# Performance work log

Measured on AMD Instinct MI355X. Metric: run time of the kernel, lower is better.

The kernel has to match this reference:

```python
import jax, jax.numpy as jnp
import numpy as np

N_NODES = 40000
N_EDGES = 320000
IN_C = 256
OUT_C = 256
K = 5


def setup_inputs() -> dict:
    key = jax.random.key(0)
    k1, k2, k3, k4, k5 = jax.random.split(key, 5)
    x = jax.random.normal(k1, (N_NODES, IN_C), dtype=jnp.float32)
    edge_index = jax.random.randint(k2, (2, N_EDGES), 0, N_NODES, dtype=jnp.int64)
    edge_weight = jax.random.uniform(k3, (N_EDGES,), dtype=jnp.float32)
    # parameters: uniform(-stdv, stdv) with stdv = 1/sqrt(in_channels * K)
    stdv = 1.0 / np.sqrt(IN_C * K)
    weight = jax.random.uniform(k4, (K, IN_C, OUT_C), dtype=jnp.float32,
                                minval=-stdv, maxval=stdv)
    bias = jax.random.uniform(k5, (OUT_C,), dtype=jnp.float32,
                              minval=-stdv, maxval=stdv)
    return {"x": x, "edge_index": edge_index, "edge_weight": edge_weight,
            "weight": weight, "bias": bias}


def reference(x, edge_index, edge_weight, weight, bias):
    row, col = edge_index[0], edge_index[1]
    num_nodes = x.shape[0]
    k_order = weight.shape[0]

    # remove_self_loops: mask out row==col edges (static-shape equivalent)
    keep = (row != col)
    ew = jnp.where(keep, edge_weight, 0.0)

    # degree over rows (counting only non-self-loop edges), D^{-1/2}
    deg = jax.ops.segment_sum(keep.astype(x.dtype), row, num_segments=num_nodes)
    deg_inv_sqrt = jnp.where(deg > 0, jax.lax.rsqrt(jnp.maximum(deg, 1.0)), 0.0)

    # scaled Laplacian edge values: -d_r^{-1/2} * w * d_c^{-1/2}
    lap = -deg_inv_sqrt[row] * ew * deg_inv_sqrt[col]

    def spmm(v):  # [N, C] -> [N, C] : scatter-add of lap-weighted gathered rows
        return jax.ops.segment_sum(lap[:, None] * v[col], row, num_segments=num_nodes)

    # Chebyshev recursion: T0 = x, T1 = L x, T_k = 2 L T_{k-1} - T_{k-2}
    tx0 = x
    out = tx0 @ weight[0]
    if k_order > 1:
        tx1 = spmm(x)
        out = out + tx1 @ weight[1]
        for k in range(2, k_order):
            tx2 = 2.0 * spmm(tx1) - tx0
            out = out + tx2 @ weight[k]
            tx0, tx1 = tx1, tx2
    return out + bias
```

## Files before the change

kernel.cpp:

```cpp
#include <hip/hip_runtime.h>

#define NN 40000
#define NE 320000
#define C 256
#define KORD 5
#define KT 1280

typedef __attribute__((ext_vector_type(8))) short short8;
typedef __attribute__((ext_vector_type(4))) float floatx4;
typedef unsigned short bf16_t;
typedef unsigned long long u64;

__device__ __forceinline__ bf16_t f2bf(float f) {
    union { float f; unsigned u; } v; v.f = f;
    unsigned r = v.u + 0x7fffu + ((v.u >> 16) & 1u);
    return (bf16_t)(r >> 16);
}
__device__ __forceinline__ float bf2f(bf16_t h) {
    union { unsigned u; float f; } v; v.u = ((unsigned)h) << 16;
    return v.f;
}

#define GLL16(gsrc, ldst)                                                        \
    __builtin_amdgcn_global_load_lds(                                            \
        (const __attribute__((address_space(1))) void*)(gsrc),                   \
        (__attribute__((address_space(3))) void*)(ldst), 16, 0, 0)

__global__ __launch_bounds__(256)
void mega0_kernel(const int* __restrict__ ei,
                  int* __restrict__ self_cnt,
                  const float* __restrict__ x, bf16_t* __restrict__ abf,
                  const float* __restrict__ W, bf16_t* __restrict__ WT) {
    int bid = blockIdx.x, t = threadIdx.x;
    if (bid < 1250) {
        int e = bid * 256 + t;
        int r = ei[e];
        int c = ei[NE + e];
        atomicAdd(&self_cnt[NN + r], 1);
        if (r == c) atomicAdd(&self_cnt[r], 1);
    } else if (bid < 11250) {
        int i = (bid - 1250) * 256 + t;
        int n = i >> 6, cg = i & 63;
        float4 f = *(const float4*)&x[(size_t)n * C + cg * 4];
        ushort4 h;
        h.x = f2bf(f.x); h.y = f2bf(f.y); h.z = f2bf(f.z); h.w = f2bf(f.w);
        *(ushort4*)&abf[(size_t)n * KT + cg * 4] = h;
    } else {
        int i = (bid - 11250) * 256 + t;
        int n = i & 255, kt = i >> 8;
        WT[(size_t)n * KT + kt] = f2bf(W[(size_t)kt * 256 + n]);
    }
}

__global__ void scan1_kernel(const int* __restrict__ cnt,
                             int* __restrict__ incl,
                             int* __restrict__ bsum) {
    __shared__ int s[256];
    int t = threadIdx.x;
    int idx = blockIdx.x * 256 + t;
    int v = (idx < NN) ? cnt[idx] : 0;
    s[t] = v;
    __syncthreads();
    for (int off = 1; off < 256; off <<= 1) {
        int add = (t >= off) ? s[t - off] : 0;
        __syncthreads();
        s[t] += add;
        __syncthreads();
    }
    if (idx < NN) incl[idx] = s[t];
    if (t == 255) bsum[blockIdx.x] = s[255];
}

__global__ void scan3_kernel(const int* __restrict__ self_cnt,
                             const int* __restrict__ incl,
                             const int* __restrict__ bsum,
                             float* __restrict__ dis,
                             int* __restrict__ row_ptr,
                             int* __restrict__ cursor) {
    __shared__ int ws[4];
    int bid = blockIdx.x, t = threadIdx.x;
    int v = (t < bid) ? bsum[t] : 0;
#pragma unroll
    for (int off = 32; off >= 1; off >>= 1) v += __shfl_down(v, off);
    if ((t & 63) == 0) ws[t >> 6] = v;
    __syncthreads();
    int bexcl = ws[0] + ws[1] + ws[2] + ws[3];
    int idx = bid * 256 + t;
    if (idx == 0) row_ptr[NN] = NE;
    if (idx >= NN) return;
    int cv = self_cnt[NN + idx];
    int rp = incl[idx] - cv + bexcl;
    row_ptr[idx] = rp;
    cursor[idx]  = rp;
    int d = cv - self_cnt[idx];
    dis[idx] = (d > 0) ? rsqrtf((float)d) : 0.0f;
}

__global__ void fill_kernel(const int* __restrict__ ei,
                            const float* __restrict__ ew,
                            const float* __restrict__ dis,
                            int* __restrict__ cursor,
                            u64* __restrict__ csr) {
    int e = blockIdx.x * 256 + threadIdx.x;
    if (e >= NE) return;
    int r = ei[e];
    int c = ei[NE + e];
    int pos = atomicAdd(&cursor[r], 1);
    float w = (r != c) ? ew[e] : 0.0f;
    float v = -dis[r] * w * dis[c];
    union { float f; unsigned u; } vb; vb.f = v;
    csr[pos] = ((u64)vb.u << 32) | (unsigned)c;
}

__global__ __launch_bounds__(256)
void spmm_kernel(const bf16_t* __restrict__ Vb,
                 const bf16_t* __restrict__ subb,
                 const int* __restrict__ row_ptr,
                 const u64* __restrict__ csr,
                 bf16_t* __restrict__ outb,
                 float alpha, int use_sub) {
    int wave = __builtin_amdgcn_readfirstlane(threadIdx.x >> 6);
    int lane = threadIdx.x & 63;
    int n = blockIdx.x * 4 + wave;
    int j0 = row_ptr[n];
    int j1 = row_ptr[n + 1];
    int cb = lane * 4;
    float a0 = 0.f, a1 = 0.f, a2 = 0.f, a3 = 0.f;
    int j = j0;
    for (; j + 8 <= j1; j += 8) {
        u64 pp[8]; ushort4 vv[8];
#pragma unroll
        for (int u = 0; u < 8; ++u) pp[u] = csr[j + u];
#pragma unroll
        for (int u = 0; u < 8; ++u)
            vv[u] = *(const ushort4*)&Vb[(size_t)(unsigned)(pp[u] & 0xffffffffu) * KT + cb];
#pragma unroll
        for (int u = 0; u < 8; ++u) {
            union { unsigned u; float f; } wb; wb.u = (unsigned)(pp[u] >> 32);
            float w = wb.f;
            a0 += w * bf2f(vv[u].x); a1 += w * bf2f(vv[u].y);
            a2 += w * bf2f(vv[u].z); a3 += w * bf2f(vv[u].w);
        }
    }
    for (; j + 4 <= j1; j += 4) {
        u64 pp[4]; ushort4 vv[4];
#pragma unroll
        for (int u = 0; u < 4; ++u) pp[u] = csr[j + u];
#pragma unroll
        for (int u = 0; u < 4; ++u)
            vv[u] = *(const ushort4*)&Vb[(size_t)(unsigned)(pp[u] & 0xffffffffu) * KT + cb];
#pragma unroll
        for (int u = 0; u < 4; ++u) {
            union { unsigned u; float f; } wb; wb.u = (unsigned)(pp[u] >> 32);
            float w = wb.f;
            a0 += w * bf2f(vv[u].x); a1 += w * bf2f(vv[u].y);
            a2 += w * bf2f(vv[u].z); a3 += w * bf2f(vv[u].w);
        }
    }
    for (; j < j1; ++j) {
        u64 pk = csr[j];
        union { unsigned u; float f; } wb; wb.u = (unsigned)(pk >> 32);
        float w = wb.f;
        ushort4 v = *(const ushort4*)&Vb[(size_t)(unsigned)(pk & 0xffffffffu) * KT + cb];
        a0 += w * bf2f(v.x); a1 += w * bf2f(v.y);
        a2 += w * bf2f(v.z); a3 += w * bf2f(v.w);
    }
    float r0, r1, r2, r3;
    if (use_sub) {
        ushort4 s = *(const ushort4*)&subb[(size_t)n * KT + cb];
        r0 = alpha * a0 - bf2f(s.x);
        r1 = alpha * a1 - bf2f(s.y);
        r2 = alpha * a2 - bf2f(s.z);
        r3 = alpha * a3 - bf2f(s.w);
    } else {
        r0 = alpha * a0; r1 = alpha * a1; r2 = alpha * a2; r3 = alpha * a3;
    }
    ushort4 h;
    h.x = f2bf(r0); h.y = f2bf(r1); h.z = f2bf(r2); h.w = f2bf(r3);
    *(ushort4*)&outb[(size_t)n * KT + cb] = h;
}

__global__ __launch_bounds__(256, 2)
void gemm_mfma(const bf16_t* __restrict__ Abf,
               const bf16_t* __restrict__ WT,
               const float* __restrict__ bias,
               float* __restrict__ out) {
    __shared__ bf16_t smem[3][12288];
    int tid = threadIdx.x;
    int w = tid >> 6, lane = tid & 63;
    int m0 = blockIdx.x * 64;
    int n0 = blockIdx.y * 128;
    int wm = w & 1, wn = w >> 1;
    int quad = lane >> 4, l16 = lane & 15, l7 = l16 & 7;

    const bf16_t* srcbase[6];
#pragma unroll
    for (int j = 0; j < 6; ++j) {
        int gi = (w * 6 + j) * 64 + lane;
        int isB = gi >= 512;
        int t  = isB ? gi - 512 : gi;
        int row = t >> 3;
        int pg = t & 7;
        int g  = pg ^ (row & 7);
        srcbase[j] = (isB ? WT + (size_t)(n0 + row) * KT
                          : Abf + (size_t)(m0 + row) * KT) + g * 8;
    }

    int arowb = wm * 32 + l16;
    int browb = wn * 64 + l16;

    floatx4 acc[2][4] = {};

    const int NT = KT / 64;

#pragma unroll
    for (int j = 0; j < 6; ++j)
        GLL16(srcbase[j] + 0 * 64, &smem[0][(w * 6 + j) * 512]);
#pragma unroll
    for (int j = 0; j < 6; ++j)
        GLL16(srcbase[j] + 1 * 64, &smem[1][(w * 6 + j) * 512]);

    int bufc = 0;
    for (int t = 0; t < NT; ++t) {
        if (t < NT - 1) {
            asm volatile("s_waitcnt vmcnt(6)" ::: "memory");
        } else {
            asm volatile("s_waitcnt vmcnt(0)" ::: "memory");
        }
        __builtin_amdgcn_sched_barrier(0);
        __builtin_amdgcn_s_barrier();

        if (t + 2 < NT) {
            int bnext = bufc + 2; if (bnext >= 3) bnext -= 3;
#pragma unroll
            for (int j = 0; j < 6; ++j)
                GLL16(srcbase[j] + (t + 2) * 64, &smem[bnext][(w * 6 + j) * 512]);
        }

        const bf16_t* sb = smem[bufc];
#pragma unroll
        for (int c = 0; c < 2; ++c) {
            int gp   = (c * 4 + quad) ^ l7;
            int aoff = (arowb * 8 + gp) * 8;
            int boff = 4096 + (browb * 8 + gp) * 8;
            short8 af[2], bfr[4];
#pragma unroll
            for (int mt = 0; mt < 2; ++mt) af[mt]  = *(const short8*)&sb[aoff + mt * 1024];
#pragma unroll
            for (int nt = 0; nt < 4; ++nt) bfr[nt] = *(const short8*)&sb[boff + nt * 1024];
#pragma unroll
            for (int mt = 0; mt < 2; ++mt)
#pragma unroll
                for (int nt = 0; nt < 4; ++nt)
                    acc[mt][nt] = __builtin_amdgcn_mfma_f32_16x16x32_bf16(
                        af[mt], bfr[nt], acc[mt][nt], 0, 0, 0);
        }

        bufc += 1; if (bufc == 3) bufc = 0;
    }

#pragma unroll
    for (int nt = 0; nt < 4; ++nt) {
        int n = n0 + wn * 64 + nt * 16 + l16;
        float bv = bias[n];
#pragma unroll
        for (int mt = 0; mt < 2; ++mt) {
            int mbase = m0 + wm * 32 + mt * 16 + quad * 4;
#pragma unroll
            for (int r = 0; r < 4; ++r)
                out[(size_t)(mbase + r) * C + n] = acc[mt][nt][r] + bv;
        }
    }
}


extern "C" void kernel_launch(void* const* d_in, const int* in_sizes, int n_in,
                              void* d_out, int out_size, void* d_ws, size_t ws_size,
                              hipStream_t stream) {
    const float* x    = (const float*)d_in[0];
    const int*   ei   = (const int*)d_in[1];
    const float* ew   = (const float*)d_in[2];
    const float* W    = (const float*)d_in[3];
    const float* bias = (const float*)d_in[4];
    float* out = (float*)d_out;

    char* p = (char*)d_ws;
    auto carve = [&](size_t bytes) {
        char* q = p;
        p += (bytes + 255) & ~(size_t)255;
        return q;
    };
    int*    self_cnt = (int*)  carve(NN * 4 * 2);
    int*    incl    = (int*)   carve(NN * 4);
    int*    bsum    = (int*)   carve(256 * 4);
    int*    row_ptr = (int*)   carve((NN + 1) * 4);
    int*    cursor  = (int*)   carve(NN * 4);
    u64*    csr     = (u64*)   carve((size_t)NE * 8);
    float*  dis     = (float*) carve(NN * 4);
    bf16_t* abf     = (bf16_t*)carve((size_t)NN * KT * 2);
    bf16_t* WT      = (bf16_t*)carve((size_t)C * KT * 2);
    (void)ws_size; (void)n_in; (void)in_sizes; (void)out_size;

    const int NB_E = (NE + 255) / 256;
    const int NB_N = (NN + 255) / 256;

    hipMemsetAsync(self_cnt, 0, NN * 4 * 2, stream);

    mega0_kernel<<<12530, 256, 0, stream>>>(ei, self_cnt, x, abf, W, WT);

    scan1_kernel<<<NB_N, 256, 0, stream>>>(self_cnt + NN, incl, bsum);
    scan3_kernel<<<NB_N, 256, 0, stream>>>(self_cnt, incl, bsum, dis, row_ptr, cursor);
    fill_kernel<<<NB_E, 256, 0, stream>>>(ei, ew, dis, cursor, csr);

    spmm_kernel<<<NN / 4, 256, 0, stream>>>(abf + 0 * 256, nullptr, row_ptr, csr,
                                            abf + 1 * 256, 1.0f, 0);
    spmm_kernel<<<NN / 4, 256, 0, stream>>>(abf + 1 * 256, abf + 0 * 256, row_ptr,
                                            csr, abf + 2 * 256, 2.0f, 1);
    spmm_kernel<<<NN / 4, 256, 0, stream>>>(abf + 2 * 256, abf + 1 * 256, row_ptr,
                                            csr, abf + 3 * 256, 2.0f, 1);
    spmm_kernel<<<NN / 4, 256, 0, stream>>>(abf + 3 * 256, abf + 2 * 256, row_ptr,
                                            csr, abf + 4 * 256, 2.0f, 1);

    dim3 ggrid(625, 2);
    gemm_mfma<<<ggrid, 256, 0, stream>>>(abf, WT, bias, out);
}
```

Measured before the change: 282.2 us.

## Replace CSR build with fixed-width ELL layout and drop scan kernels

Replaces the count/scan/fill CSR construction with a fixed-width ELL array of 40 slots per row, indexed directly by row and an atomic cursor. This removes the two scan kernels and the row_ptr and dis arrays; the normalisation factors are now computed inside the fill kernel from the degree counts. The SpMM loop now always runs in steps of 8 over zero-padded slots (zero weight, column 0), so the remainder loops go away. In exchange, a larger workspace region (about 12.8 MB) must be memset each call, each row does some wasted padded gathers, and any row with more than 40 edges would overflow silently into the next row.

New measurement: 278.7 us. About the same (-1.3%).

```diff
diff --git a/kernel.cpp b/kernel.cpp
--- a/kernel.cpp
+++ b/kernel.cpp
@@ -5,6 +5,7 @@
 #define C 256
 #define KORD 5
 #define KT 1280
+#define ELLW 40
 
 typedef __attribute__((ext_vector_type(8))) short short8;
 typedef __attribute__((ext_vector_type(4))) float floatx4;
@@ -28,7 +29,7 @@
 
 __global__ __launch_bounds__(256)
 void mega0_kernel(const int* __restrict__ ei,
-                  int* __restrict__ self_cnt,
+                  int* __restrict__ self, int* __restrict__ cntA,
                   const float* __restrict__ x, bf16_t* __restrict__ abf,
                   const float* __restrict__ W, bf16_t* __restrict__ WT) {
     int bid = blockIdx.x, t = threadIdx.x;
@@ -36,8 +37,8 @@
         int e = bid * 256 + t;
         int r = ei[e];
         int c = ei[NE + e];
-        atomicAdd(&self_cnt[NN + r], 1);
-        if (r == c) atomicAdd(&self_cnt[r], 1);
+        atomicAdd(&cntA[r], 1);
+        if (r == c) atomicAdd(&self[r], 1);
     } else if (bid < 11250) {
         int i = (bid - 1250) * 256 + t;
         int n = i >> 6, cg = i & 63;
@@ -52,85 +53,46 @@
     }
 }
 
-__global__ void scan1_kernel(const int* __restrict__ cnt,
-                             int* __restrict__ incl,
-                             int* __restrict__ bsum) {
-    __shared__ int s[256];
-    int t = threadIdx.x;
-    int idx = blockIdx.x * 256 + t;
-    int v = (idx < NN) ? cnt[idx] : 0;
-    s[t] = v;
-    __syncthreads();
-    for (int off = 1; off < 256; off <<= 1) {
-        int add = (t >= off) ? s[t - off] : 0;
-        __syncthreads();
-        s[t] += add;
-        __syncthreads();
-    }
-    if (idx < NN) incl[idx] = s[t];
-    if (t == 255) bsum[blockIdx.x] = s[255];
-}
-
-__global__ void scan3_kernel(const int* __restrict__ self_cnt,
-                             const int* __restrict__ incl,
-                             const int* __restrict__ bsum,
-                             float* __restrict__ dis,
-                             int* __restrict__ row_ptr,
-                             int* __restrict__ cursor) {
-    __shared__ int ws[4];
-    int bid = blockIdx.x, t = threadIdx.x;
-    int v = (t < bid) ? bsum[t] : 0;
-#pragma unroll
-    for (int off = 32; off >= 1; off >>= 1) v += __shfl_down(v, off);
-    if ((t & 63) == 0) ws[t >> 6] = v;
-    __syncthreads();
-    int bexcl = ws[0] + ws[1] + ws[2] + ws[3];
-    int idx = bid * 256 + t;
-    if (idx == 0) row_ptr[NN] = NE;
-    if (idx >= NN) return;
-    int cv = self_cnt[NN + idx];
-    int rp = incl[idx] - cv + bexcl;
-    row_ptr[idx] = rp;
-    cursor[idx]  = rp;
-    int d = cv - self_cnt[idx];
-    dis[idx] = (d > 0) ? rsqrtf((float)d) : 0.0f;
-}
-
-__global__ void fill_kernel(const int* __restrict__ ei,
-                            const float* __restrict__ ew,
-                            const float* __restrict__ dis,
-                            int* __restrict__ cursor,
-                            u64* __restrict__ csr) {
+__global__ __launch_bounds__(256)
+void fill_kernel(const int* __restrict__ ei,
+                 const float* __restrict__ ew,
+                 const int* __restrict__ self,
+                 const int* __restrict__ cntA,
+                 int* __restrict__ cur,
+                 u64* __restrict__ ell) {
     int e = blockIdx.x * 256 + threadIdx.x;
     if (e >= NE) return;
     int r = ei[e];
     int c = ei[NE + e];
-    int pos = atomicAdd(&cursor[r], 1);
+    int pos = atomicAdd(&cur[r], 1);
     float w = (r != c) ? ew[e] : 0.0f;
-    float v = -dis[r] * w * dis[c];
+    int dgr = cntA[r] - self[r];
+    int dgc = cntA[c] - self[c];
+    float dr = (dgr > 0) ? rsqrtf((float)dgr) : 0.0f;
+    float dc = (dgc > 0) ? rsqrtf((float)dgc) : 0.0f;
+    float v = -dr * w * dc;
     union { float f; unsigned u; } vb; vb.f = v;
-    csr[pos] = ((u64)vb.u << 32) | (unsigned)c;
+    ell[(size_t)r * ELLW + pos] = ((u64)vb.u << 32) | (unsigned)c;
 }
 
 __global__ __launch_bounds__(256)
 void spmm_kernel(const bf16_t* __restrict__ Vb,
                  const bf16_t* __restrict__ subb,
-                 const int* __restrict__ row_ptr,
-                 const u64* __restrict__ csr,
+                 const int* __restrict__ cntA,
+                 const u64* __restrict__ ell,
                  bf16_t* __restrict__ outb,
                  float alpha, int use_sub) {
     int wave = __builtin_amdgcn_readfirstlane(threadIdx.x >> 6);
     int lane = threadIdx.x & 63;
     int n = blockIdx.x * 4 + wave;
-    int j0 = row_ptr[n];
-    int j1 = row_ptr[n + 1];
+    const u64* row = ell + (size_t)n * ELLW;
+    int jmax = (cntA[n] + 7) & ~7;
     int cb = lane * 4;
     float a0 = 0.f, a1 = 0.f, a2 = 0.f, a3 = 0.f;
-    int j = j0;
-    for (; j + 8 <= j1; j += 8) {
+    for (int j = 0; j < jmax; j += 8) {
         u64 pp[8]; ushort4 vv[8];
 #pragma unroll
-        for (int u = 0; u < 8; ++u) pp[u] = csr[j + u];
+        for (int u = 0; u < 8; ++u) pp[u] = row[j + u];
 #pragma unroll
         for (int u = 0; u < 8; ++u)
             vv[u] = *(const ushort4*)&Vb[(size_t)(unsigned)(pp[u] & 0xffffffffu) * KT + cb];
@@ -141,29 +103,6 @@
             a0 += w * bf2f(vv[u].x); a1 += w * bf2f(vv[u].y);
             a2 += w * bf2f(vv[u].z); a3 += w * bf2f(vv[u].w);
         }
-    }
-    for (; j + 4 <= j1; j += 4) {
-        u64 pp[4]; ushort4 vv[4];
-#pragma unroll
-        for (int u = 0; u < 4; ++u) pp[u] = csr[j + u];
-#pragma unroll
-        for (int u = 0; u < 4; ++u)
-            vv[u] = *(const ushort4*)&Vb[(size_t)(unsigned)(pp[u] & 0xffffffffu) * KT + cb];
-#pragma unroll
-        for (int u = 0; u < 4; ++u) {
-            union { unsigned u; float f; } wb; wb.u = (unsigned)(pp[u] >> 32);
-            float w = wb.f;
-            a0 += w * bf2f(vv[u].x); a1 += w * bf2f(vv[u].y);
-            a2 += w * bf2f(vv[u].z); a3 += w * bf2f(vv[u].w);
-        }
-    }
-    for (; j < j1; ++j) {
-        u64 pk = csr[j];
-        union { unsigned u; float f; } wb; wb.u = (unsigned)(pk >> 32);
-        float w = wb.f;
-        ushort4 v = *(const ushort4*)&Vb[(size_t)(unsigned)(pk & 0xffffffffu) * KT + cb];
-        a0 += w * bf2f(v.x); a1 += w * bf2f(v.y);
-        a2 += w * bf2f(v.z); a3 += w * bf2f(v.w);
     }
     float r0, r1, r2, r3;
     if (use_sub) {
@@ -290,36 +229,30 @@
         p += (bytes + 255) & ~(size_t)255;
         return q;
     };
-    int*    self_cnt = (int*)  carve(NN * 4 * 2);
-    int*    incl    = (int*)   carve(NN * 4);
-    int*    bsum    = (int*)   carve(256 * 4);
-    int*    row_ptr = (int*)   carve((NN + 1) * 4);
-    int*    cursor  = (int*)   carve(NN * 4);
-    u64*    csr     = (u64*)   carve((size_t)NE * 8);
-    float*  dis     = (float*) carve(NN * 4);
+    int*    self    = (int*)   carve(NN * 4);
+    int*    cntA    = (int*)   carve(NN * 4);
+    int*    cur     = (int*)   carve(NN * 4);
+    u64*    ell     = (u64*)   carve((size_t)NN * ELLW * 8);
     bf16_t* abf     = (bf16_t*)carve((size_t)NN * KT * 2);
     bf16_t* WT      = (bf16_t*)carve((size_t)C * KT * 2);
     (void)ws_size; (void)n_in; (void)in_sizes; (void)out_size;
 
     const int NB_E = (NE + 255) / 256;
-    const int NB_N = (NN + 255) / 256;
-
-    hipMemsetAsync(self_cnt, 0, NN * 4 * 2, stream);
-
-    mega0_kernel<<<12530, 256, 0, stream>>>(ei, self_cnt, x, abf, W, WT);
-
-    scan1_kernel<<<NB_N, 256, 0, stream>>>(self_cnt + NN, incl, bsum);
-    scan3_kernel<<<NB_N, 256, 0, stream>>>(self_cnt, incl, bsum, dis, row_ptr, cursor);
-    fill_kernel<<<NB_E, 256, 0, stream>>>(ei, ew, dis, cursor, csr);
-
-    spmm_kernel<<<NN / 4, 256, 0, stream>>>(abf + 0 * 256, nullptr, row_ptr, csr,
+
+    hipMemsetAsync(self, 0, (size_t)NN * 4 * 3 + (size_t)NN * ELLW * 8, stream);
+
+    mega0_kernel<<<12530, 256, 0, stream>>>(ei, self, cntA, x, abf, W, WT);
+
+    fill_kernel<<<NB_E, 256, 0, stream>>>(ei, ew, self, cntA, cur, ell);
+
+    spmm_kernel<<<NN / 4, 256, 0, stream>>>(abf + 0 * 256, nullptr, cntA, ell,
                                             abf + 1 * 256, 1.0f, 0);
-    spmm_kernel<<<NN / 4, 256, 0, stream>>>(abf + 1 * 256, abf + 0 * 256, row_ptr,
-                                            csr, abf + 2 * 256, 2.0f, 1);
-    spmm_kernel<<<NN / 4, 256, 0, stream>>>(abf + 2 * 256, abf + 1 * 256, row_ptr,
-                                            csr, abf + 3 * 256, 2.0f, 1);
-    spmm_kernel<<<NN / 4, 256, 0, stream>>>(abf + 3 * 256, abf + 2 * 256, row_ptr,
-                                            csr, abf + 4 * 256, 2.0f, 1);
+    spmm_kernel<<<NN / 4, 256, 0, stream>>>(abf + 1 * 256, abf + 0 * 256, cntA, ell,
+                                            abf + 2 * 256, 2.0f, 1);
+    spmm_kernel<<<NN / 4, 256, 0, stream>>>(abf + 2 * 256, abf + 1 * 256, cntA, ell,
+                                            abf + 3 * 256, 2.0f, 1);
+    spmm_kernel<<<NN / 4, 256, 0, stream>>>(abf + 3 * 256, abf + 2 * 256, cntA, ell,
+                                            abf + 4 * 256, 2.0f, 1);
 
     dim3 ggrid(625, 2);
     gemm_mfma<<<ggrid, 256, 0, stream>>>(abf, WT, bias, out);
```
